# Optimization experiments

Measured on AMD Instinct MI355X. Metric: run time of the kernel, lower is better.

Reference implementation:

```python
import jax, jax.numpy as jnp
import numpy as np

HEADS = 8
DIM_HEAD = 64
SCALE = DIM_HEAD ** (-0.5)


def setup_inputs() -> dict:
    key = jax.random.key(0)
    k1, k2, k3 = jax.random.split(key, 3)
    b, dim, w = 8, 256, 2048
    hidden = HEADS * DIM_HEAD  # 512
    x = jax.random.normal(k1, (b, dim, w), dtype=jnp.float32)
    # Conv1d kernel-size-1 weights collapse to matrices; scale like torch init
    w_qkv = jax.random.normal(k2, (3 * hidden, dim), dtype=jnp.float32) * (1.0 / np.sqrt(dim))
    w_out = jax.random.normal(k3, (dim, hidden), dtype=jnp.float32) * (1.0 / np.sqrt(hidden))
    b_out = jnp.zeros((dim,), dtype=jnp.float32)
    return {"x": x, "w_qkv": w_qkv, "w_out": w_out, "b_out": b_out}


def reference(x, w_qkv, w_out, b_out):
    b, c, w = x.shape
    h, dh = HEADS, DIM_HEAD
    # 1x1 conv == matmul over channel dim: [3*hidden, dim] x [b, dim, w] -> [b, 3*hidden, w]
    qkv = jnp.einsum('od,bdw->bow', w_qkv, x)
    q, k, v = jnp.split(qkv, 3, axis=1)
    # 'b (h c) x -> b h c x'
    q = q.reshape(b, h, dh, w) * SCALE
    k = k.reshape(b, h, dh, w)
    v = v.reshape(b, h, dh, w)
    sim = jnp.einsum('bhdi,bhdj->bhij', q, k)          # [b, h, w, w]
    sim = sim - jax.lax.stop_gradient(sim.max(axis=-1, keepdims=True))
    attn = jax.nn.softmax(sim, axis=-1)
    out = jnp.einsum('bhij,bhdj->bhid', attn, v)        # [b, h, w, dh]
    # 'b h x c -> b (h c) x'
    out = out.transpose(0, 1, 3, 2).reshape(b, h * dh, w)
    # output 1x1 conv with bias
    return jnp.einsum('oc,bcw->bow', w_out, out) + b_out[None, :, None]
```

## Files before the change

kernel.cpp:

```cpp
#include <hip/hip_runtime.h>
#include <hip/hip_bf16.h>

typedef __bf16 bf16x8 __attribute__((ext_vector_type(8)));
typedef float f32x4 __attribute__((ext_vector_type(4)));
typedef float f32x16 __attribute__((ext_vector_type(16)));

#define MFMA16x16(a, b, c) __builtin_amdgcn_mfma_f32_16x16x32_bf16((a), (b), (c), 0, 0, 0)
#define MFMA32x32(a, b, c) __builtin_amdgcn_mfma_f32_32x32x16_bf16((a), (b), (c), 0, 0, 0)

namespace {
constexpr int BATCH = 8;
constexpr int DIMC  = 256;
constexpr int WLEN  = 2048;
constexpr int DH    = 64;
constexpr int HID   = 512;
constexpr float QSCALE = 0.125f * 1.44269504088896340736f;

constexpr size_t OFF_WQKV = 0;
constexpr size_t OFF_WOUT = 786432;
constexpr size_t OFF_XT   = 1048576;
constexpr size_t OFF_QKT  = 9437184;
constexpr size_t OFF_V    = 42991616;
constexpr size_t OFF_AT   = 59768832;
}

__device__ inline unsigned cvt_pk_bf16(float a, float b) {
  unsigned r;
  asm("v_cvt_pk_bf16_f32 %0, %1, %2" : "=v"(r) : "v"(a), "v"(b));
  return r;
}

__device__ inline void permswap(unsigned &a, unsigned &b) {
  asm("v_permlane32_swap_b32 %0, %1" : "+v"(a), "+v"(b));
}

union U4 { unsigned u[4]; bf16x8 v; };

__device__ inline float softmax_half(const f32x16 st, bf16x8 &pfa, bf16x8 &pfb) {
  float e[16];
#pragma unroll
  for (int r = 0; r < 16; ++r) e[r] = __builtin_amdgcn_exp2f(st[r]);
  float t0 = (e[0] + e[1]) + (e[2] + e[3]);
  float t1 = (e[4] + e[5]) + (e[6] + e[7]);
  float t2 = (e[8] + e[9]) + (e[10] + e[11]);
  float t3 = (e[12] + e[13]) + (e[14] + e[15]);
  float rs = (t0 + t1) + (t2 + t3);
  unsigned w[8];
#pragma unroll
  for (int q = 0; q < 8; ++q) w[q] = cvt_pk_bf16(e[2 * q], e[2 * q + 1]);
  unsigned a0 = w[0], a1 = w[1], a2 = w[2], a3 = w[3];
  permswap(a0, a2);
  permswap(a1, a3);
  U4 ua; ua.u[0] = a0; ua.u[1] = a1; ua.u[2] = a2; ua.u[3] = a3;
  pfa = ua.v;
  unsigned b0 = w[4], b1 = w[5], b2 = w[6], b3 = w[7];
  permswap(b0, b2);
  permswap(b1, b3);
  U4 ub; ub.u[0] = b0; ub.u[1] = b1; ub.u[2] = b2; ub.u[3] = b3;
  pfb = ub.v;
  return rs;
}

__global__ __launch_bounds__(256) void prep_weights(
    const float* __restrict__ wqkv, const float* __restrict__ wout,
    __hip_bfloat16* __restrict__ wqkv_bf, __hip_bfloat16* __restrict__ wout_bf) {
  int i = blockIdx.x * 256 + threadIdx.x;
  if (i < 1536 * 256) wqkv_bf[i] = __float2bfloat16(wqkv[i]);
  if (i < 256 * 512)  wout_bf[i] = __float2bfloat16(wout[i]);
}

__global__ __launch_bounds__(256) void transpose_x(
    const float* __restrict__ x, __hip_bfloat16* __restrict__ xT) {
  __shared__ float t[64][65];
  int b = blockIdx.z;
  int d0 = blockIdx.y * 64, w0 = blockIdx.x * 64;
  int tid = threadIdx.x;
  const float* xb = x + (size_t)b * DIMC * WLEN;
#pragma unroll
  for (int r = 0; r < 16; ++r) {
    int dd = r * 4 + (tid >> 6);
    int ww = tid & 63;
    t[dd][ww] = xb[(size_t)(d0 + dd) * WLEN + w0 + ww];
  }
  __syncthreads();
  __hip_bfloat16* xTb = xT + (size_t)b * WLEN * DIMC;
#pragma unroll
  for (int r = 0; r < 16; ++r) {
    int ww = r * 4 + (tid >> 6);
    int dd = tid & 63;
    xTb[(size_t)(w0 + ww) * DIMC + d0 + dd] = __float2bfloat16(t[dd][ww]);
  }
}

__global__ __launch_bounds__(256) void qkv_gemm(
    const __hip_bfloat16* __restrict__ wqkv_bf,
    const __hip_bfloat16* __restrict__ xT,
    __hip_bfloat16* __restrict__ qkT, __hip_bfloat16* __restrict__ vbuf) {
  int b = blockIdx.z;
  int o0 = blockIdx.y * 128, w0 = blockIdx.x * 128;
  int tid = threadIdx.x;
  int wid = tid >> 6, lane = tid & 63;
  int il = lane & 31, hi = lane >> 5;
  int wo = (wid >> 1) * 64;
  int ww = (wid & 1) * 64;

  __shared__ __align__(16) char lds_raw[36864];
  __hip_bfloat16* Al = reinterpret_cast<__hip_bfloat16*>(lds_raw);
  __hip_bfloat16* Bl = Al + 2 * 128 * 36;

  const __hip_bfloat16* xb = xT + (size_t)b * WLEN * DIMC;

  const int srow = tid >> 2;
  const int scol = (tid & 3) * 8;
  const __hip_bfloat16* asrc = wqkv_bf + (size_t)(o0 + srow) * DIMC + scol;
  const __hip_bfloat16* bsrc = xb + (size_t)(w0 + srow) * DIMC + scol;

  bf16x8 ga0, ga1, gb0, gb1;
  auto stage_load = [&](int k0) {
    ga0 = *reinterpret_cast<const bf16x8*>(asrc + k0);
    ga1 = *reinterpret_cast<const bf16x8*>(asrc + 64 * DIMC + k0);
    gb0 = *reinterpret_cast<const bf16x8*>(bsrc + k0);
    gb1 = *reinterpret_cast<const bf16x8*>(bsrc + 64 * DIMC + k0);
  };
  auto stage_write = [&](int bf) {
    *reinterpret_cast<bf16x8*>(Al + (bf * 128 + srow) * 36 + scol)      = ga0;
    *reinterpret_cast<bf16x8*>(Al + (bf * 128 + srow + 64) * 36 + scol) = ga1;
    *reinterpret_cast<bf16x8*>(Bl + (bf * 128 + srow) * 36 + scol)      = gb0;
    *reinterpret_cast<bf16x8*>(Bl + (bf * 128 + srow + 64) * 36 + scol) = gb1;
  };

  f32x16 acc[2][2];
#pragma unroll
  for (int ta = 0; ta < 2; ++ta)
#pragma unroll
    for (int tb = 0; tb < 2; ++tb)
#pragma unroll
      for (int r = 0; r < 16; ++r) acc[ta][tb][r] = 0.f;

  auto compute = [&](int cur) {
    bf16x8 af[2][2], bfr[2][2];
#pragma unroll
    for (int ta = 0; ta < 2; ++ta)
#pragma unroll
      for (int kk = 0; kk < 2; ++kk) {
        af[ta][kk] = *reinterpret_cast<const bf16x8*>(
            Al + (cur * 128 + wo + ta * 32 + il) * 36 + kk * 16 + hi * 8);
        bfr[ta][kk] = *reinterpret_cast<const bf16x8*>(
            Bl + (cur * 128 + ww + ta * 32 + il) * 36 + kk * 16 + hi * 8);
      }
    __builtin_amdgcn_s_setprio(1);
#pragma unroll
    for (int kk = 0; kk < 2; ++kk)
#pragma unroll
      for (int ta = 0; ta < 2; ++ta)
#pragma unroll
        for (int tb = 0; tb < 2; ++tb)
          acc[ta][tb] = MFMA32x32(af[ta][kk], bfr[tb][kk], acc[ta][tb]);
    __builtin_amdgcn_s_setprio(0);
  };

  stage_load(0);
  stage_write(0);
  __syncthreads();
#pragma unroll 1
  for (int t = 0; t < 7; ++t) {
    stage_load((t + 1) * 32);
    compute(t & 1);
    stage_write((t + 1) & 1);
    __syncthreads();
  }
  compute(1);
  __syncthreads();

  if (o0 < 1024) {
    float scale = (o0 < 512) ? QSCALE : 1.0f;
    __hip_bfloat16* bw = reinterpret_cast<__hip_bfloat16*>(lds_raw);
#pragma unroll
    for (int ta = 0; ta < 2; ++ta)
#pragma unroll
      for (int tb = 0; tb < 2; ++tb)
#pragma unroll
        for (int q = 0; q < 8; ++q) {
          int dl = ((2 * q) & 3) + 8 * (q >> 1) + 4 * hi;
          int row = ww + tb * 32 + il;
          int col = wo + ta * 32 + dl;
          unsigned pk = cvt_pk_bf16(acc[ta][tb][2 * q] * scale,
                                    acc[ta][tb][2 * q + 1] * scale);
          *reinterpret_cast<unsigned*>(bw + row * 136 + col) = pk;
        }
    __syncthreads();
    __hip_bfloat16* outq = qkT + (size_t)b * WLEN * 1024;
#pragma unroll
    for (int it = 0; it < 8; ++it) {
      int row = it * 16 + (tid >> 4);
      int c = (tid & 15) * 8;
      bf16x8 v = *reinterpret_cast<const bf16x8*>(bw + row * 136 + c);
      *reinterpret_cast<bf16x8*>(outq + (size_t)(w0 + row) * 1024 + o0 + c) = v;
    }
  } else {
    __hip_bfloat16* bo = reinterpret_cast<__hip_bfloat16*>(lds_raw);
#pragma unroll
    for (int ta = 0; ta < 2; ++ta)
#pragma unroll
      for (int tb = 0; tb < 2; ++tb)
#pragma unroll
        for (int r = 0; r < 16; ++r) {
          int orow = wo + ta * 32 + (r & 3) + 8 * (r >> 2) + 4 * hi;
          int wcol = ww + tb * 32 + il;
          bo[orow * 136 + wcol] = __float2bfloat16(acc[ta][tb][r]);
        }
    __syncthreads();
    __hip_bfloat16* outv = vbuf + (size_t)b * HID * WLEN;
#pragma unroll
    for (int it = 0; it < 8; ++it) {
      int orow = it * 16 + (tid >> 4);
      int c = (tid & 15) * 8;
      bf16x8 v = *reinterpret_cast<const bf16x8*>(bo + orow * 136 + c);
      *reinterpret_cast<bf16x8*>(outv + (size_t)(o0 - 1024 + orow) * WLEN + w0 + c) = v;
    }
  }
}

__global__ __launch_bounds__(256) void attn_kernel(
    const __hip_bfloat16* __restrict__ qkT,
    const __hip_bfloat16* __restrict__ vbuf,
    __hip_bfloat16* __restrict__ attnT) {
  int f = blockIdx.x;
  int xcd = f & 7, slot = f >> 3;
  int b = slot >> 4;
  int h = xcd;
  int xb = slot & 15;
  int tid = threadIdx.x, wid = tid >> 6, lane = tid & 63;
  int il = lane & 31, hi = lane >> 5;
  int i0w = xb * 128 + wid * 32;

  const __hip_bfloat16* qk_b = qkT + (size_t)b * WLEN * 1024;
  const __hip_bfloat16* vb = vbuf + (size_t)b * HID * WLEN + (size_t)h * DH * WLEN;

  __shared__ __align__(16) __hip_bfloat16 Kl[2][64][72];
  __shared__ __align__(16) __hip_bfloat16 Vl[2][64][72];

  bf16x8 qf[4];
  {
    const __hip_bfloat16* qrow = qk_b + (size_t)(i0w + il) * 1024 + h * 64 + hi * 8;
#pragma unroll
    for (int s = 0; s < 4; ++s)
      qf[s] = *reinterpret_cast<const bf16x8*>(qrow + s * 16);
  }

  f32x16 oacc0, oacc1;
#pragma unroll
  for (int r = 0; r < 16; ++r) { oacc0[r] = 0.f; oacc1[r] = 0.f; }
  float l_lane = 0.f;

  const int srow = tid >> 3;
  const int scol = (tid & 7) * 8;
  const __hip_bfloat16* ksrc = qk_b + 512 + h * 64 + scol;
  const __hip_bfloat16* vsrc = vb + scol;

  bf16x8 gk0, gk1, gv0, gv1;
  auto stage_load = [&](int j0) {
    gk0 = *reinterpret_cast<const bf16x8*>(ksrc + (size_t)(j0 + srow) * 1024);
    gk1 = *reinterpret_cast<const bf16x8*>(ksrc + (size_t)(j0 + srow + 32) * 1024);
    gv0 = *reinterpret_cast<const bf16x8*>(vsrc + (size_t)srow * WLEN + j0);
    gv1 = *reinterpret_cast<const bf16x8*>(vsrc + (size_t)(srow + 32) * WLEN + j0);
  };
  auto stage_write = [&](int bf) {
    *reinterpret_cast<bf16x8*>(&Kl[bf][srow][scol])      = gk0;
    *reinterpret_cast<bf16x8*>(&Kl[bf][srow + 32][scol]) = gk1;
    *reinterpret_cast<bf16x8*>(&Vl[bf][srow][scol])      = gv0;
    *reinterpret_cast<bf16x8*>(&Vl[bf][srow + 32][scol]) = gv1;
  };

  auto compute = [&](int cur) {
    f32x16 st0, st1;
#pragma unroll
    for (int r = 0; r < 16; ++r) { st0[r] = 0.f; st1[r] = 0.f; }
    __builtin_amdgcn_s_setprio(1);
#pragma unroll
    for (int s = 0; s < 4; ++s)
      st0 = MFMA32x32(*reinterpret_cast<const bf16x8*>(&Kl[cur][il][s * 16 + hi * 8]),
                      qf[s], st0);
#pragma unroll
    for (int s = 0; s < 4; ++s)
      st1 = MFMA32x32(*reinterpret_cast<const bf16x8*>(&Kl[cur][il + 32][s * 16 + hi * 8]),
                      qf[s], st1);
    __builtin_amdgcn_s_setprio(0);

    bf16x8 p0, p1, p2, p3;
    l_lane += softmax_half(st0, p0, p1);
    l_lane += softmax_half(st1, p2, p3);

    __builtin_amdgcn_s_setprio(1);
    oacc0 = MFMA32x32(*reinterpret_cast<const bf16x8*>(&Vl[cur][il][hi * 8]),      p0, oacc0);
    oacc1 = MFMA32x32(*reinterpret_cast<const bf16x8*>(&Vl[cur][il + 32][hi * 8]), p0, oacc1);
    oacc0 = MFMA32x32(*reinterpret_cast<const bf16x8*>(&Vl[cur][il][16 + hi * 8]),      p1, oacc0);
    oacc1 = MFMA32x32(*reinterpret_cast<const bf16x8*>(&Vl[cur][il + 32][16 + hi * 8]), p1, oacc1);
    oacc0 = MFMA32x32(*reinterpret_cast<const bf16x8*>(&Vl[cur][il][32 + hi * 8]),      p2, oacc0);
    oacc1 = MFMA32x32(*reinterpret_cast<const bf16x8*>(&Vl[cur][il + 32][32 + hi * 8]), p2, oacc1);
    oacc0 = MFMA32x32(*reinterpret_cast<const bf16x8*>(&Vl[cur][il][48 + hi * 8]),      p3, oacc0);
    oacc1 = MFMA32x32(*reinterpret_cast<const bf16x8*>(&Vl[cur][il + 32][48 + hi * 8]), p3, oacc1);
    __builtin_amdgcn_s_setprio(0);
  };

  stage_load(0);
  stage_write(0);
  __syncthreads();

  constexpr int NT = WLEN / 64;
#pragma unroll 1
  for (int t = 0; t < NT - 1; ++t) {
    stage_load((t + 1) * 64);
    compute(t & 1);
    stage_write((t + 1) & 1);
    __syncthreads();
  }
  compute((NT - 1) & 1);
  __syncthreads();

  float l = l_lane + __shfl_xor(l_lane, 32);
  __hip_bfloat16* olds = &Kl[0][0][0];
  float rl = 1.0f / l;
#pragma unroll
  for (int q = 0; q < 8; ++q) {
    int dl = ((2 * q) & 3) + 8 * (q >> 1) + 4 * hi;
    unsigned pk0 = cvt_pk_bf16(oacc0[2 * q] * rl, oacc0[2 * q + 1] * rl);
    unsigned pk1 = cvt_pk_bf16(oacc1[2 * q] * rl, oacc1[2 * q + 1] * rl);
    *reinterpret_cast<unsigned*>(olds + (wid * 32 + il) * 72 + dl)      = pk0;
    *reinterpret_cast<unsigned*>(olds + (wid * 32 + il) * 72 + 32 + dl) = pk1;
  }
  __hip_bfloat16* ob = attnT + (size_t)b * WLEN * HID + h * 64;
  int dcol = (lane & 7) * 8;
#pragma unroll
  for (int it = 0; it < 4; ++it) {
    int ir = it * 8 + (lane >> 3);
    bf16x8 vrow = *reinterpret_cast<const bf16x8*>(olds + (wid * 32 + ir) * 72 + dcol);
    *reinterpret_cast<bf16x8*>(ob + (size_t)(i0w + ir) * HID + dcol) = vrow;
  }
}

__global__ __launch_bounds__(256) void out_proj(
    const __hip_bfloat16* __restrict__ attnT,
    const __hip_bfloat16* __restrict__ wout_bf,
    const float* __restrict__ b_out, float* __restrict__ out) {
  int b = blockIdx.z;
  int o0 = blockIdx.y * 128, w0 = blockIdx.x * 64;
  int tid = threadIdx.x;
  int wid = tid >> 6, lane = tid & 63;
  int il = lane & 31, hi = lane >> 5;
  int wo = (wid >> 1) * 64;
  int ww = (wid & 1) * 32;

  __shared__ __align__(16) __hip_bfloat16 Al[2][128][36];
  __shared__ __align__(16) __hip_bfloat16 Bl[2][64][36];

  const __hip_bfloat16* at_b = attnT + (size_t)b * WLEN * HID;

  const int srow = tid >> 2;
  const int scol = (tid & 3) * 8;
  const __hip_bfloat16* asrc = wout_bf + (size_t)(o0 + srow) * HID + scol;
  const __hip_bfloat16* bsrc = at_b + (size_t)(w0 + srow) * HID + scol;

  bf16x8 ga0, ga1, gb0;
  auto stage_load = [&](int k0) {
    ga0 = *reinterpret_cast<const bf16x8*>(asrc + k0);
    ga1 = *reinterpret_cast<const bf16x8*>(asrc + 64 * HID + k0);
    gb0 = *reinterpret_cast<const bf16x8*>(bsrc + k0);
  };
  auto stage_write = [&](int bf) {
    *reinterpret_cast<bf16x8*>(&Al[bf][srow][scol])      = ga0;
    *reinterpret_cast<bf16x8*>(&Al[bf][srow + 64][scol]) = ga1;
    *reinterpret_cast<bf16x8*>(&Bl[bf][srow][scol])      = gb0;
  };

  f32x16 acc[2];
#pragma unroll
  for (int ta = 0; ta < 2; ++ta)
#pragma unroll
    for (int r = 0; r < 16; ++r) acc[ta][r] = 0.f;

  auto compute = [&](int cur) {
    bf16x8 af[2][2], bfr[2];
#pragma unroll
    for (int kk = 0; kk < 2; ++kk) {
      bfr[kk] = *reinterpret_cast<const bf16x8*>(&Bl[cur][ww + il][kk * 16 + hi * 8]);
#pragma unroll
      for (int ta = 0; ta < 2; ++ta)
        af[ta][kk] = *reinterpret_cast<const bf16x8*>(
            &Al[cur][wo + ta * 32 + il][kk * 16 + hi * 8]);
    }
    __builtin_amdgcn_s_setprio(1);
#pragma unroll
    for (int kk = 0; kk < 2; ++kk)
#pragma unroll
      for (int ta = 0; ta < 2; ++ta)
        acc[ta] = MFMA32x32(af[ta][kk], bfr[kk], acc[ta]);
    __builtin_amdgcn_s_setprio(0);
  };

  stage_load(0);
  stage_write(0);
  __syncthreads();
#pragma unroll 1
  for (int t = 0; t < 15; ++t) {
    stage_load((t + 1) * 32);
    compute(t & 1);
    stage_write((t + 1) & 1);
    __syncthreads();
  }
  compute(1);

  float* outb = out + (size_t)b * DIMC * WLEN;
#pragma unroll
  for (int ta = 0; ta < 2; ++ta)
#pragma unroll
    for (int r = 0; r < 16; ++r) {
      int og = o0 + wo + ta * 32 + (r & 3) + 8 * (r >> 2) + 4 * hi;
      int wg = w0 + ww + il;
      outb[(size_t)og * WLEN + wg] = acc[ta][r] + b_out[og];
    }
}

extern "C" void kernel_launch(void* const* d_in, const int* in_sizes, int n_in,
                              void* d_out, int out_size, void* d_ws, size_t ws_size,
                              hipStream_t stream) {
  const float* x    = (const float*)d_in[0];
  const float* wqkv = (const float*)d_in[1];
  const float* wout = (const float*)d_in[2];
  const float* bout = (const float*)d_in[3];
  float* out = (float*)d_out;
  char* ws = (char*)d_ws;

  __hip_bfloat16* wqkv_bf = (__hip_bfloat16*)(ws + OFF_WQKV);
  __hip_bfloat16* wout_bf = (__hip_bfloat16*)(ws + OFF_WOUT);
  __hip_bfloat16* xT      = (__hip_bfloat16*)(ws + OFF_XT);
  __hip_bfloat16* qkT     = (__hip_bfloat16*)(ws + OFF_QKT);
  __hip_bfloat16* vbuf    = (__hip_bfloat16*)(ws + OFF_V);
  __hip_bfloat16* attnT   = (__hip_bfloat16*)(ws + OFF_AT);

  prep_weights<<<dim3(1536), dim3(256), 0, stream>>>(wqkv, wout, wqkv_bf, wout_bf);
  transpose_x<<<dim3(WLEN / 64, DIMC / 64, BATCH), dim3(256), 0, stream>>>(x, xT);
  qkv_gemm<<<dim3(WLEN / 128, 1536 / 128, BATCH), dim3(256), 0, stream>>>(wqkv_bf, xT, qkT, vbuf);
  attn_kernel<<<dim3(1024), dim3(256), 0, stream>>>(qkT, vbuf, attnT);
  out_proj<<<dim3(WLEN / 64, DIMC / 128, BATCH), dim3(256), 0, stream>>>(attnT, wout_bf, bout, out);
}
```

Before: 185.7 us.

## Merge weight prep into x transpose kernel, unroll main loops, interleave QK MFMAs

```diff
diff --git a/kernel.cpp b/kernel.cpp
--- a/kernel.cpp
+++ b/kernel.cpp
@@ -61,20 +61,28 @@
   return rs;
 }
 
-__global__ __launch_bounds__(256) void prep_weights(
-    const float* __restrict__ wqkv, const float* __restrict__ wout,
+__global__ __launch_bounds__(256) void prep_transpose(
+    const float* __restrict__ x, const float* __restrict__ wqkv,
+    const float* __restrict__ wout, __hip_bfloat16* __restrict__ xT,
     __hip_bfloat16* __restrict__ wqkv_bf, __hip_bfloat16* __restrict__ wout_bf) {
-  int i = blockIdx.x * 256 + threadIdx.x;
-  if (i < 1536 * 256) wqkv_bf[i] = __float2bfloat16(wqkv[i]);
-  if (i < 256 * 512)  wout_bf[i] = __float2bfloat16(wout[i]);
-}
-
-__global__ __launch_bounds__(256) void transpose_x(
-    const float* __restrict__ x, __hip_bfloat16* __restrict__ xT) {
+  int tid = threadIdx.x;
+  if (blockIdx.z == 8) {
+    int flat = (blockIdx.y * 32 + blockIdx.x) * 256 + tid;
+#pragma unroll
+    for (int it = 0; it < 12; ++it) {
+      int i = it * 32768 + flat;
+      wqkv_bf[i] = __float2bfloat16(wqkv[i]);
+    }
+#pragma unroll
+    for (int it = 0; it < 4; ++it) {
+      int i = it * 32768 + flat;
+      wout_bf[i] = __float2bfloat16(wout[i]);
+    }
+    return;
+  }
   __shared__ float t[64][65];
   int b = blockIdx.z;
   int d0 = blockIdx.y * 64, w0 = blockIdx.x * 64;
-  int tid = threadIdx.x;
   const float* xb = x + (size_t)b * DIMC * WLEN;
 #pragma unroll
   for (int r = 0; r < 16; ++r) {
@@ -162,7 +170,7 @@
   stage_load(0);
   stage_write(0);
   __syncthreads();
-#pragma unroll 1
+#pragma unroll 2
   for (int t = 0; t < 7; ++t) {
     stage_load((t + 1) * 32);
     compute(t & 1);
@@ -248,9 +256,9 @@
       qf[s] = *reinterpret_cast<const bf16x8*>(qrow + s * 16);
   }
 
-  f32x16 oacc0, oacc1;
-#pragma unroll
-  for (int r = 0; r < 16; ++r) { oacc0[r] = 0.f; oacc1[r] = 0.f; }
+  f32x16 oacc0, oacc1, fzero;
+#pragma unroll
+  for (int r = 0; r < 16; ++r) { oacc0[r] = 0.f; oacc1[r] = 0.f; fzero[r] = 0.f; }
   float l_lane = 0.f;
 
   const int srow = tid >> 3;
@@ -274,17 +282,20 @@
 
   auto compute = [&](int cur) {
     f32x16 st0, st1;
-#pragma unroll
-    for (int r = 0; r < 16; ++r) { st0[r] = 0.f; st1[r] = 0.f; }
     __builtin_amdgcn_s_setprio(1);
-#pragma unroll
-    for (int s = 0; s < 4; ++s)
-      st0 = MFMA32x32(*reinterpret_cast<const bf16x8*>(&Kl[cur][il][s * 16 + hi * 8]),
-                      qf[s], st0);
-#pragma unroll
-    for (int s = 0; s < 4; ++s)
-      st1 = MFMA32x32(*reinterpret_cast<const bf16x8*>(&Kl[cur][il + 32][s * 16 + hi * 8]),
-                      qf[s], st1);
+    {
+      bf16x8 k0 = *reinterpret_cast<const bf16x8*>(&Kl[cur][il][hi * 8]);
+      bf16x8 k1 = *reinterpret_cast<const bf16x8*>(&Kl[cur][il + 32][hi * 8]);
+      st0 = MFMA32x32(k0, qf[0], fzero);
+      st1 = MFMA32x32(k1, qf[0], fzero);
+    }
+#pragma unroll
+    for (int s = 1; s < 4; ++s) {
+      bf16x8 k0 = *reinterpret_cast<const bf16x8*>(&Kl[cur][il][s * 16 + hi * 8]);
+      bf16x8 k1 = *reinterpret_cast<const bf16x8*>(&Kl[cur][il + 32][s * 16 + hi * 8]);
+      st0 = MFMA32x32(k0, qf[s], st0);
+      st1 = MFMA32x32(k1, qf[s], st1);
+    }
     __builtin_amdgcn_s_setprio(0);
 
     bf16x8 p0, p1, p2, p3;
@@ -308,7 +319,7 @@
   __syncthreads();
 
   constexpr int NT = WLEN / 64;
-#pragma unroll 1
+#pragma unroll 2
   for (int t = 0; t < NT - 1; ++t) {
     stage_load((t + 1) * 64);
     compute(t & 1);
@@ -401,7 +412,7 @@
   stage_load(0);
   stage_write(0);
   __syncthreads();
-#pragma unroll 1
+#pragma unroll 2
   for (int t = 0; t < 15; ++t) {
     stage_load((t + 1) * 32);
     compute(t & 1);
@@ -438,8 +449,8 @@
   __hip_bfloat16* vbuf    = (__hip_bfloat16*)(ws + OFF_V);
   __hip_bfloat16* attnT   = (__hip_bfloat16*)(ws + OFF_AT);
 
-  prep_weights<<<dim3(1536), dim3(256), 0, stream>>>(wqkv, wout, wqkv_bf, wout_bf);
-  transpose_x<<<dim3(WLEN / 64, DIMC / 64, BATCH), dim3(256), 0, stream>>>(x, xT);
+  prep_transpose<<<dim3(WLEN / 64, DIMC / 64, 9), dim3(256), 0, stream>>>(
+      x, wqkv, wout, xT, wqkv_bf, wout_bf);
   qkv_gemm<<<dim3(WLEN / 128, 1536 / 128, BATCH), dim3(256), 0, stream>>>(wqkv_bf, xT, qkT, vbuf);
   attn_kernel<<<dim3(1024), dim3(256), 0, stream>>>(qkT, vbuf, attnT);
   out_proj<<<dim3(WLEN / 64, DIMC / 128, BATCH), dim3(256), 0, stream>>>(attnT, wout_bf, bout, out);
```

Measured after the change: 168.9 us. 1.1x faster.
